# Kernel optimization log

Hardware: AMD Instinct MI355X
Metric: run time of the kernel (lower is better)

The kernel has to match this reference:

```python
import jax, jax.numpy as jnp
import numpy as np
from jax import lax

B = 32
NUM_CLASSES = 80
NUM_ANCHORS = 3
IMG_SIZE = 320
STRIDES = (8, 16, 32)
TOPK = 1000
CONF_THRESH = 0.05
NMS_THRESH = 0.6
EPS = 1e-10

ANCHOR_SIZES = np.array([[16, 16], [32, 32], [64, 48],
                         [64, 64], [96, 96], [128, 96],
                         [128, 128], [192, 160], [256, 256]],
                        dtype=np.float32).reshape(3, NUM_ANCHORS, 2)


def _build_anchors():
    # mirrors YOWOv3.generate_anchors
    boxes, strides = [], []
    for lvl, s in enumerate(STRIDES):
        f = IMG_SIZE // s
        ys, xs = np.meshgrid(np.arange(f), np.arange(f), indexing='ij')
        xy = np.stack([xs, ys], axis=-1).astype(np.float32).reshape(-1, 1, 2)
        xy = np.repeat(xy, NUM_ANCHORS, axis=1) * s            # [f*f, A, 2]
        wh = np.broadcast_to(ANCHOR_SIZES[lvl], (f * f, NUM_ANCHORS, 2))
        boxes.append(np.concatenate([xy, wh], axis=-1).reshape(-1, 4))
        strides.append(np.full(f * f * NUM_ANCHORS, s, dtype=np.float32))
    return np.concatenate(boxes, 0), np.concatenate(strides, 0)


def setup_inputs() -> dict:
    key = jax.random.key(0)
    k1, k2, k3 = jax.random.split(key, 3)
    anchors_np, stride_np = _build_anchors()
    M = anchors_np.shape[0]  # 6300
    conf_pred = jax.random.normal(k1, (B, M, 1), dtype=jnp.float32)
    cls_pred = jax.random.normal(k2, (B, M, NUM_CLASSES), dtype=jnp.float32) * 2.0
    reg_pred = jax.random.normal(k3, (B, M, 4), dtype=jnp.float32) * 0.5
    return {
        'conf_pred': conf_pred,
        'cls_pred': cls_pred,
        'reg_pred': reg_pred,
        'anchors': jnp.asarray(anchors_np),
        'stride_map': jnp.asarray(stride_np),
    }


def _decode_boxes(anchors, stride_map, reg_pred):
    # anchors [M,4] (cx, cy, w, h) in pixels; reg_pred [B,M,4]
    ctr = anchors[None, :, :2] + jax.nn.sigmoid(reg_pred[..., :2]) * stride_map[None, :, None]
    wh = anchors[None, :, 2:] * jnp.exp(reg_pred[..., 2:])
    return jnp.concatenate([ctr - 0.5 * wh, ctr + 0.5 * wh], axis=-1)  # [B,M,4] x1y1x2y2


def _nms_keep(boxes, scores, labels):
    # boxes [K,4] sorted by descending score; per-class greedy NMS -> bool keep [K]
    x1, y1, x2, y2 = boxes[:, 0], boxes[:, 1], boxes[:, 2], boxes[:, 3]
    areas = (x2 - x1) * (y2 - y1)
    xx1 = jnp.maximum(x1[:, None], x1[None, :])
    yy1 = jnp.maximum(y1[:, None], y1[None, :])
    xx2 = jnp.minimum(x2[:, None], x2[None, :])
    yy2 = jnp.minimum(y2[:, None], y2[None, :])
    inter = jnp.maximum(EPS, xx2 - xx1) * jnp.maximum(EPS, yy2 - yy1)
    union = jnp.maximum(areas[:, None] + areas[None, :] - inter, EPS)
    iou = inter / union
    suppress = (iou > NMS_THRESH) & (labels[:, None] == labels[None, :])
    keep0 = scores >= CONF_THRESH
    idxs = jnp.arange(boxes.shape[0])

    def body(i, keep):
        # if box i is kept, suppress all later same-class boxes with iou > thresh
        return keep & ~(keep[i] & suppress[i] & (idxs > i))

    return lax.fori_loop(0, boxes.shape[0], body, keep0)


def reference(conf_pred, cls_pred, reg_pred, anchors, stride_map):
    box_pred = _decode_boxes(anchors, stride_map, reg_pred)              # [B,M,4]
    joint = jax.nn.sigmoid(conf_pred) * jax.nn.softmax(cls_pred, -1)     # [B,M,C]
    scores = jnp.max(joint, axis=-1)                                     # [B,M]
    labels = jnp.argmax(joint, axis=-1)                                  # [B,M]

    top_scores, top_idx = lax.top_k(scores, TOPK)                        # sorted desc
    top_labels = jnp.take_along_axis(labels, top_idx, axis=1)
    top_boxes = jnp.take_along_axis(box_pred, top_idx[..., None], axis=1)
    top_boxes = jnp.clip(top_boxes / IMG_SIZE, 0.0, 1.0)                 # [B,K,4]

    keep = jax.vmap(_nms_keep)(top_boxes, top_scores, top_labels)        # [B,K] bool
    return top_scores, top_labels, top_boxes, keep
```

## Files before the change

kernel.cpp:

```cpp
#include <hip/hip_runtime.h>
#include <stdint.h>

#define NB 32
#define NM 6300
#define NC 80
#define NTOP 1000
#define NPAD 1024
#define NCAND 2048
#define NBINS 4096
#define BDT 1024

static constexpr float IMGSZ   = 320.0f;
static constexpr float CONF_TH = 0.05f;
static constexpr float NMS_TH  = 0.6f;
static constexpr float EPSF    = 1e-10f;

static constexpr size_t OFF_SCORES = 0;
static constexpr size_t OFF_LABELS = OFF_SCORES + (size_t)NB * NM * 4;
static constexpr size_t OFF_NBOX   = OFF_LABELS + (size_t)NB * NM * 4;
static constexpr size_t OFF_NLAB   = OFF_NBOX   + (size_t)NB * NPAD * 16;
static constexpr size_t OFF_SUP    = ((OFF_NLAB + (size_t)NB * NPAD * 4) + 1023) & ~(size_t)1023;

__global__ __launch_bounds__(256) void k_score(const float* __restrict__ conf,
                                               const float* __restrict__ cls,
                                               float* __restrict__ scores,
                                               int* __restrict__ labels) {
#pragma clang fp contract(off)
    int t = blockIdx.x * blockDim.x + threadIdx.x;
    int a = t >> 4;
    int l = t & 15;
    if (a >= NB * NM) return;
    const float* row = cls + (size_t)a * NC;

    float v[5];
#pragma unroll
    for (int k = 0; k < 5; ++k) v[k] = row[l + 16 * k];

    float bv = v[0];
    int bi = l;
#pragma unroll
    for (int k = 1; k < 5; ++k) {
        int c = l + 16 * k;
        if (v[k] > bv) { bv = v[k]; bi = c; }
    }
#pragma unroll
    for (int m = 1; m < 16; m <<= 1) {
        float ov = __shfl_xor(bv, m, 16);
        int   oi = __shfl_xor(bi, m, 16);
        if (ov > bv || (ov == bv && oi < bi)) { bv = ov; bi = oi; }
    }
    float s = 0.0f;
#pragma unroll
    for (int k = 0; k < 5; ++k) s += expf(v[k] - bv);
#pragma unroll
    for (int m = 1; m < 16; m <<= 1) s += __shfl_xor(s, m, 16);

    if (l == 0) {
        float cf  = conf[a];
        float sig = 1.0f / (1.0f + expf(-cf));
        float inv = 1.0f / s;
        scores[a] = sig * inv;
        labels[a] = bi;
    }
}

__global__ __launch_bounds__(BDT) void k_topk(const float* __restrict__ scores,
                                              const int* __restrict__ labels,
                                              const float* __restrict__ reg,
                                              const float* __restrict__ anchors,
                                              const float* __restrict__ stridemap,
                                              float* __restrict__ out_scores,
                                              float* __restrict__ out_labels,
                                              float* __restrict__ out_boxes,
                                              float* __restrict__ nbox,
                                              int* __restrict__ nlab) {
#pragma clang fp contract(off)
    __shared__ uint32_t hist[NBINS];
    __shared__ uint64_t key[NCAND];
    __shared__ int scnt;
    __shared__ int sT;
    int b = blockIdx.x, tid = threadIdx.x;
    const float* sb = scores + (size_t)b * NM;

    for (int i = tid; i < NBINS; i += BDT) hist[i] = 0;
    for (int i = tid; i < NCAND; i += BDT) key[i] = 0;
    if (tid == 0) scnt = 0;
    __syncthreads();

    for (int i = tid; i < NM; i += BDT)
        atomicAdd(&hist[__float_as_uint(sb[i]) >> 20], 1u);
    __syncthreads();

    if (tid < 64) {
        int l = tid;
        uint32_t q = 0;
        for (int i = 0; i < 64; ++i) q += hist[l * 64 + i];
        uint32_t s = q;
        for (int off = 1; off < 64; off <<= 1) {
            uint32_t o = __shfl_down(s, off);
            if (l + off < 64) s += o;
        }
        uint64_t m = __ballot(s >= (uint32_t)NTOP);
        int c = 63 - __clzll(m);
        uint32_t sc_ = __shfl(s, c);
        uint32_t qc  = __shfl(q, c);
        uint32_t tail = sc_ - qc;
        uint32_t v = hist[c * 64 + l];
        uint32_t s2 = v;
        for (int off = 1; off < 64; off <<= 1) {
            uint32_t o = __shfl_down(s2, off);
            if (l + off < 64) s2 += o;
        }
        uint64_t m2 = __ballot(s2 + tail >= (uint32_t)NTOP);
        int T = c * 64 + (63 - __clzll(m2));
        if (l == 0) sT = T;
    }
    __syncthreads();

    uint32_t T = (uint32_t)sT;
    int lane = tid & 63;
    for (int i = tid; i < NM; i += BDT) {
        uint32_t bits = __float_as_uint(sb[i]);
        bool pred = (bits >> 20) >= T;
        uint64_t mask = __ballot(pred);
        if (pred) {
            int leader = __ffsll((unsigned long long)mask) - 1;
            int prefix = __popcll(mask & ((1ull << lane) - 1));
            int base = 0;
            if (lane == leader) base = atomicAdd(&scnt, (int)__popcll(mask));
            base = __shfl(base, leader);
            int pos = base + prefix;
            if (pos < NCAND)
                key[pos] = ((uint64_t)bits << 32) | (uint32_t)(~(uint32_t)i);
        }
    }
    __syncthreads();

    uint64_t e0 = key[tid];
    uint64_t e1 = key[tid + 1024];

#pragma unroll
    for (int kk = 2; kk <= NCAND; kk <<= 1) {
#pragma unroll
        for (int j = kk >> 1; j > 0; j >>= 1) {
            if (j == 1024) {
                uint64_t mx = (e0 >= e1) ? e0 : e1;
                uint64_t mn = (e0 >= e1) ? e1 : e0;
                e0 = mx; e1 = mn;
            } else if (j >= 64) {
                __syncthreads();
                key[tid] = e0; key[tid + 1024] = e1;
                __syncthreads();
                uint64_t o0 = key[tid ^ j];
                uint64_t o1 = key[(tid + 1024) ^ j];
                bool lo  = ((tid & j) == 0);
                bool up0 = ((tid & kk) == 0);
                bool up1 = (((tid + 1024) & kk) == 0);
                e0 = (lo == up0) ? ((e0 >= o0) ? e0 : o0) : ((e0 >= o0) ? o0 : e0);
                e1 = (lo == up1) ? ((e1 >= o1) ? e1 : o1) : ((e1 >= o1) ? o1 : e1);
            } else {
                uint64_t o0 = __shfl_xor((unsigned long long)e0, j);
                uint64_t o1 = __shfl_xor((unsigned long long)e1, j);
                bool lo  = ((lane & j) == 0);
                bool up0 = ((tid & kk) == 0);
                bool up1 = (((tid + 1024) & kk) == 0);
                e0 = (lo == up0) ? ((e0 >= o0) ? e0 : o0) : ((e0 >= o0) ? o0 : e0);
                e1 = (lo == up1) ? ((e1 >= o1) ? e1 : o1) : ((e1 >= o1) ? o1 : e1);
            }
        }
    }

    if (tid < NTOP) {
        uint32_t sbits = (uint32_t)(e0 >> 32);
        int idx = (int)(~(uint32_t)e0);
        out_scores[b * NTOP + tid] = __uint_as_float(sbits);
        int lab = labels[(size_t)b * NM + idx];
        out_labels[b * NTOP + tid] = (float)lab;

        const float* rg = reg + ((size_t)b * NM + idx) * 4;
        float rx = rg[0], ry = rg[1], rw = rg[2], rh = rg[3];
        const float* an = anchors + (size_t)idx * 4;
        float ax = an[0], ay = an[1], aw = an[2], ah = an[3];
        float st = stridemap[idx];

        float sx = 1.0f / (1.0f + expf(-rx));
        float sy = 1.0f / (1.0f + expf(-ry));
        float cx = ax + sx * st;
        float cy = ay + sy * st;
        float w  = aw * expf(rw);
        float h  = ah * expf(rh);
        float x1 = cx - 0.5f * w, y1 = cy - 0.5f * h;
        float x2 = cx + 0.5f * w, y2 = cy + 0.5f * h;

        float nx1 = fminf(fmaxf(x1 / IMGSZ, 0.0f), 1.0f);
        float ny1 = fminf(fmaxf(y1 / IMGSZ, 0.0f), 1.0f);
        float nx2 = fminf(fmaxf(x2 / IMGSZ, 0.0f), 1.0f);
        float ny2 = fminf(fmaxf(y2 / IMGSZ, 0.0f), 1.0f);

        float4 bx = make_float4(nx1, ny1, nx2, ny2);
        ((float4*)out_boxes)[b * NTOP + tid] = bx;
        ((float4*)nbox)[b * NPAD + tid]      = bx;
        nlab[b * NPAD + tid] = lab;
    }
}

__global__ __launch_bounds__(256) void k_supmat(const float* __restrict__ nbox,
                                                const int* __restrict__ nlab,
                                                uint64_t* __restrict__ sup) {
#pragma clang fp contract(off)
    int b = blockIdx.y;
    int t = blockIdx.x;
    int tj = (int)((sqrtf(8.0f * (float)t + 1.0f) - 1.0f) * 0.5f);
    while ((tj + 1) * (tj + 2) / 2 <= t) ++tj;
    while (tj * (tj + 1) / 2 > t) --tj;
    int ti = t - tj * (tj + 1) / 2;

    int lane = threadIdx.x & 63;
    int w    = threadIdx.x >> 6;

    int i = ti * 64 + lane;
    int j = tj * 64 + lane;

    float4 bi = ((const float4*)nbox)[b * NPAD + i];
    float  ai = (bi.z - bi.x) * (bi.w - bi.y);
    int    li = nlab[b * NPAD + i];
    float4 bj = ((const float4*)nbox)[b * NPAD + j];
    int    lj = nlab[b * NPAD + j];
    bool   iv = (i < NTOP);

    uint64_t mybits = 0;
#pragma unroll
    for (int u = 0; u < 16; ++u) {
        int jj = (w << 4) | u;
        float bjx = __shfl(bj.x, jj);
        float bjy = __shfl(bj.y, jj);
        float bjz = __shfl(bj.z, jj);
        float bjw = __shfl(bj.w, jj);
        int   ljv = __shfl(lj, jj);
        float ajv = (bjz - bjx) * (bjw - bjy);
        int   jg  = tj * 64 + jj;
        float xx1 = fmaxf(bi.x, bjx);
        float yy1 = fmaxf(bi.y, bjy);
        float xx2 = fminf(bi.z, bjz);
        float yy2 = fminf(bi.w, bjw);
        float inter = fmaxf(EPSF, xx2 - xx1) * fmaxf(EPSF, yy2 - yy1);
        float uni   = fmaxf(ai + ajv - inter, EPSF);
        float iou   = inter / uni;
        bool pred = (i < jg) && iv && (jg < NTOP) && (li == ljv) && (iou > NMS_TH);
        uint64_t bal = __ballot(pred);
        if (lane == jj) mybits = bal;
    }
    if ((lane >> 4) == w)
        sup[(((size_t)b * 16 + tj) * 16 + ti) * 64 + lane] = mybits;
}

__global__ __launch_bounds__(1024) void k_nms(const float* __restrict__ out_scores,
                                              const uint64_t* __restrict__ sup,
                                              float* __restrict__ out_keep) {
    __shared__ uint64_t Kw[16];
    int b    = blockIdx.x;
    int w    = threadIdx.x >> 6;
    int lane = threadIdx.x & 63;
    const uint64_t* supb = sup + (size_t)b * 16 * 16 * 64;

    uint64_t wrow[16];
#pragma unroll
    for (int ti = 0; ti < 16; ++ti)
        wrow[ti] = (ti <= w) ? supb[((size_t)w * 16 + ti) * 64 + lane] : 0ULL;

    int pos = w * 64 + lane;
    bool k0 = (pos < NTOP) && (out_scores[b * NTOP + pos] >= CONF_TH);

    uint64_t ext = 0;
#pragma unroll
    for (int s = 0; s < 16; ++s) {
        if (w == s) {
            bool cand = k0 && (ext == 0ULL);
            uint64_t wself = wrow[s];
            uint64_t alive = __ballot(cand);
            for (int it = 0; it < 64; ++it) {
                bool dead = (wself & alive) != 0ULL;
                uint64_t na = __ballot(cand && !dead);
                if (na == alive) break;
                alive = na;
            }
            if (lane == 0) Kw[s] = alive;
            if (pos < NTOP)
                out_keep[b * NTOP + pos] = ((alive >> lane) & 1ULL) ? 1.0f : 0.0f;
        }
        __syncthreads();
        if (w > s) ext |= wrow[s] & Kw[s];
    }
}

extern "C" void kernel_launch(void* const* d_in, const int* in_sizes, int n_in,
                              void* d_out, int out_size, void* d_ws, size_t ws_size,
                              hipStream_t stream) {
    const float* conf = (const float*)d_in[0];
    const float* cls  = (const float*)d_in[1];
    const float* reg  = (const float*)d_in[2];
    const float* anch = (const float*)d_in[3];
    const float* strm = (const float*)d_in[4];

    float* out        = (float*)d_out;
    float* out_scores = out;
    float* out_labels = out + NB * NTOP;
    float* out_boxes  = out + 2 * NB * NTOP;
    float* out_keep   = out + 2 * NB * NTOP + NB * NTOP * 4;

    char* ws = (char*)d_ws;
    float*    scores = (float*)(ws + OFF_SCORES);
    int*      labels = (int*)(ws + OFF_LABELS);
    float*    nbox   = (float*)(ws + OFF_NBOX);
    int*      nlab   = (int*)(ws + OFF_NLAB);
    uint64_t* sup    = (uint64_t*)(ws + OFF_SUP);

    k_score<<<(NB * NM * 16) / 256, 256, 0, stream>>>(conf, cls, scores, labels);
    k_topk<<<NB, BDT, 0, stream>>>(scores, labels, reg, anch, strm,
                                   out_scores, out_labels, out_boxes, nbox, nlab);
    k_supmat<<<dim3(136, NB), 256, 0, stream>>>(nbox, nlab, sup);
    k_nms<<<NB, 1024, 0, stream>>>(out_scores, sup, out_keep);
}
```

Measured before the change: 67.73 us.

## Replace bitonic sort in top-k with bucket-chain rank computation

The 2048-element bitonic sort after radix-histogram thresholding is replaced. The kernel now builds a suffix-sum over histogram bins and per-bin linked lists of candidates, and computes each candidate's exact rank as the suffix count plus a walk over its own bin's chain. This removes the many __syncthreads-heavy sort stages, but adds per-candidate linked-list traversal with scattered global reads. That traversal can be slow if many candidates share a bin, and because the lists are built with atomics the chain order is nondeterministic.

```diff
diff --git a/kernel.cpp b/kernel.cpp
--- a/kernel.cpp
+++ b/kernel.cpp
@@ -8,7 +8,6 @@
 #define NPAD 1024
 #define NCAND 2048
 #define NBINS 4096
-#define BDT 1024
 
 static constexpr float IMGSZ   = 320.0f;
 static constexpr float CONF_TH = 0.05f;
@@ -64,143 +63,119 @@
     }
 }
 
-__global__ __launch_bounds__(BDT) void k_topk(const float* __restrict__ scores,
-                                              const int* __restrict__ labels,
-                                              const float* __restrict__ reg,
-                                              const float* __restrict__ anchors,
-                                              const float* __restrict__ stridemap,
-                                              float* __restrict__ out_scores,
-                                              float* __restrict__ out_labels,
-                                              float* __restrict__ out_boxes,
-                                              float* __restrict__ nbox,
-                                              int* __restrict__ nlab) {
+__global__ __launch_bounds__(1024) void k_topk(const float* __restrict__ scores,
+                                               const int* __restrict__ labels,
+                                               const float* __restrict__ reg,
+                                               const float* __restrict__ anchors,
+                                               const float* __restrict__ stridemap,
+                                               float* __restrict__ out_scores,
+                                               float* __restrict__ out_labels,
+                                               float* __restrict__ out_boxes,
+                                               float* __restrict__ nbox,
+                                               int* __restrict__ nlab) {
 #pragma clang fp contract(off)
     __shared__ uint32_t hist[NBINS];
-    __shared__ uint64_t key[NCAND];
-    __shared__ int scnt;
-    __shared__ int sT;
+    __shared__ uint32_t suf[NBINS];
+    __shared__ int      binHead[NBINS];
+    __shared__ uint16_t nxt[NM];
+    __shared__ uint16_t candList[NCAND];
+    __shared__ uint32_t csuf[64];
+    __shared__ int sT, scnt;
+
     int b = blockIdx.x, tid = threadIdx.x;
     const float* sb = scores + (size_t)b * NM;
 
-    for (int i = tid; i < NBINS; i += BDT) hist[i] = 0;
-    for (int i = tid; i < NCAND; i += BDT) key[i] = 0;
+    for (int i = tid; i < NBINS; i += 1024) { hist[i] = 0; binHead[i] = -1; }
     if (tid == 0) scnt = 0;
     __syncthreads();
 
-    for (int i = tid; i < NM; i += BDT)
+    for (int i = tid; i < NM; i += 1024)
         atomicAdd(&hist[__float_as_uint(sb[i]) >> 20], 1u);
     __syncthreads();
 
     if (tid < 64) {
-        int l = tid;
-        uint32_t q = 0;
-        for (int i = 0; i < 64; ++i) q += hist[l * 64 + i];
-        uint32_t s = q;
+        uint32_t cs = 0;
+        for (int k = 0; k < 64; ++k) cs += hist[tid * 64 + k];
+        uint32_t s = cs;
         for (int off = 1; off < 64; off <<= 1) {
             uint32_t o = __shfl_down(s, off);
-            if (l + off < 64) s += o;
-        }
-        uint64_t m = __ballot(s >= (uint32_t)NTOP);
-        int c = 63 - __clzll(m);
-        uint32_t sc_ = __shfl(s, c);
-        uint32_t qc  = __shfl(q, c);
-        uint32_t tail = sc_ - qc;
-        uint32_t v = hist[c * 64 + l];
-        uint32_t s2 = v;
+            if (tid + off < 64) s += o;
+        }
+        csuf[tid] = s - cs;
+    }
+    __syncthreads();
+
+    int ln = tid & 63, wv = tid >> 6;
+    for (int c = wv; c < 64; c += 16) {
+        uint32_t h = hist[c * 64 + ln];
+        uint32_t s = h;
         for (int off = 1; off < 64; off <<= 1) {
-            uint32_t o = __shfl_down(s2, off);
-            if (l + off < 64) s2 += o;
-        }
-        uint64_t m2 = __ballot(s2 + tail >= (uint32_t)NTOP);
-        int T = c * 64 + (63 - __clzll(m2));
-        if (l == 0) sT = T;
-    }
-    __syncthreads();
-
+            uint32_t o = __shfl_down(s, off);
+            if (ln + off < 64) s += o;
+        }
+        uint32_t sufv = csuf[c] + (s - h);
+        suf[c * 64 + ln] = sufv;
+        if (sufv < (uint32_t)NTOP && sufv + h >= (uint32_t)NTOP)
+            sT = c * 64 + ln;
+    }
+    __syncthreads();
     uint32_t T = (uint32_t)sT;
-    int lane = tid & 63;
-    for (int i = tid; i < NM; i += BDT) {
+
+    for (int i = tid; i < NM; i += 1024) {
+        uint32_t bin = __float_as_uint(sb[i]) >> 20;
+        if (bin >= T) {
+            int prev = atomicExch(&binHead[bin], i);
+            nxt[i] = (uint16_t)(prev < 0 ? 0xFFFFu : (uint32_t)prev);
+            int p = atomicAdd(&scnt, 1);
+            if (p < NCAND) candList[p] = (uint16_t)i;
+        }
+    }
+    __syncthreads();
+
+    int C = scnt; if (C > NCAND) C = NCAND;
+    for (int c = tid; c < C; c += 1024) {
+        int i = candList[c];
         uint32_t bits = __float_as_uint(sb[i]);
-        bool pred = (bits >> 20) >= T;
-        uint64_t mask = __ballot(pred);
-        if (pred) {
-            int leader = __ffsll((unsigned long long)mask) - 1;
-            int prefix = __popcll(mask & ((1ull << lane) - 1));
-            int base = 0;
-            if (lane == leader) base = atomicAdd(&scnt, (int)__popcll(mask));
-            base = __shfl(base, leader);
-            int pos = base + prefix;
-            if (pos < NCAND)
-                key[pos] = ((uint64_t)bits << 32) | (uint32_t)(~(uint32_t)i);
-        }
-    }
-    __syncthreads();
-
-    uint64_t e0 = key[tid];
-    uint64_t e1 = key[tid + 1024];
-
-#pragma unroll
-    for (int kk = 2; kk <= NCAND; kk <<= 1) {
-#pragma unroll
-        for (int j = kk >> 1; j > 0; j >>= 1) {
-            if (j == 1024) {
-                uint64_t mx = (e0 >= e1) ? e0 : e1;
-                uint64_t mn = (e0 >= e1) ? e1 : e0;
-                e0 = mx; e1 = mn;
-            } else if (j >= 64) {
-                __syncthreads();
-                key[tid] = e0; key[tid + 1024] = e1;
-                __syncthreads();
-                uint64_t o0 = key[tid ^ j];
-                uint64_t o1 = key[(tid + 1024) ^ j];
-                bool lo  = ((tid & j) == 0);
-                bool up0 = ((tid & kk) == 0);
-                bool up1 = (((tid + 1024) & kk) == 0);
-                e0 = (lo == up0) ? ((e0 >= o0) ? e0 : o0) : ((e0 >= o0) ? o0 : e0);
-                e1 = (lo == up1) ? ((e1 >= o1) ? e1 : o1) : ((e1 >= o1) ? o1 : e1);
-            } else {
-                uint64_t o0 = __shfl_xor((unsigned long long)e0, j);
-                uint64_t o1 = __shfl_xor((unsigned long long)e1, j);
-                bool lo  = ((lane & j) == 0);
-                bool up0 = ((tid & kk) == 0);
-                bool up1 = (((tid + 1024) & kk) == 0);
-                e0 = (lo == up0) ? ((e0 >= o0) ? e0 : o0) : ((e0 >= o0) ? o0 : e0);
-                e1 = (lo == up1) ? ((e1 >= o1) ? e1 : o1) : ((e1 >= o1) ? o1 : e1);
+        uint32_t bin  = bits >> 20;
+        uint32_t rank = suf[bin];
+        for (int m = binHead[bin]; m >= 0; ) {
+            if (m != i) {
+                uint32_t mb = __float_as_uint(sb[m]);
+                if (mb > bits || (mb == bits && m < i)) ++rank;
             }
-        }
-    }
-
-    if (tid < NTOP) {
-        uint32_t sbits = (uint32_t)(e0 >> 32);
-        int idx = (int)(~(uint32_t)e0);
-        out_scores[b * NTOP + tid] = __uint_as_float(sbits);
-        int lab = labels[(size_t)b * NM + idx];
-        out_labels[b * NTOP + tid] = (float)lab;
-
-        const float* rg = reg + ((size_t)b * NM + idx) * 4;
-        float rx = rg[0], ry = rg[1], rw = rg[2], rh = rg[3];
-        const float* an = anchors + (size_t)idx * 4;
-        float ax = an[0], ay = an[1], aw = an[2], ah = an[3];
-        float st = stridemap[idx];
-
-        float sx = 1.0f / (1.0f + expf(-rx));
-        float sy = 1.0f / (1.0f + expf(-ry));
-        float cx = ax + sx * st;
-        float cy = ay + sy * st;
-        float w  = aw * expf(rw);
-        float h  = ah * expf(rh);
-        float x1 = cx - 0.5f * w, y1 = cy - 0.5f * h;
-        float x2 = cx + 0.5f * w, y2 = cy + 0.5f * h;
-
-        float nx1 = fminf(fmaxf(x1 / IMGSZ, 0.0f), 1.0f);
-        float ny1 = fminf(fmaxf(y1 / IMGSZ, 0.0f), 1.0f);
-        float nx2 = fminf(fmaxf(x2 / IMGSZ, 0.0f), 1.0f);
-        float ny2 = fminf(fmaxf(y2 / IMGSZ, 0.0f), 1.0f);
-
-        float4 bx = make_float4(nx1, ny1, nx2, ny2);
-        ((float4*)out_boxes)[b * NTOP + tid] = bx;
-        ((float4*)nbox)[b * NPAD + tid]      = bx;
-        nlab[b * NPAD + tid] = lab;
+            uint16_t nx = nxt[m];
+            m = (nx == 0xFFFFu) ? -1 : (int)nx;
+        }
+        if (rank < (uint32_t)NTOP) {
+            out_scores[b * NTOP + rank] = __uint_as_float(bits);
+            int lab = labels[(size_t)b * NM + i];
+            out_labels[b * NTOP + rank] = (float)lab;
+
+            const float* rg = reg + ((size_t)b * NM + i) * 4;
+            float rx = rg[0], ry = rg[1], rw = rg[2], rh = rg[3];
+            const float* an = anchors + (size_t)i * 4;
+            float ax = an[0], ay = an[1], aw = an[2], ah = an[3];
+            float st = stridemap[i];
+
+            float sx = 1.0f / (1.0f + expf(-rx));
+            float sy = 1.0f / (1.0f + expf(-ry));
+            float cx = ax + sx * st;
+            float cy = ay + sy * st;
+            float w  = aw * expf(rw);
+            float h  = ah * expf(rh);
+            float x1 = cx - 0.5f * w, y1 = cy - 0.5f * h;
+            float x2 = cx + 0.5f * w, y2 = cy + 0.5f * h;
+
+            float nx1 = fminf(fmaxf(x1 / IMGSZ, 0.0f), 1.0f);
+            float ny1 = fminf(fmaxf(y1 / IMGSZ, 0.0f), 1.0f);
+            float nx2 = fminf(fmaxf(x2 / IMGSZ, 0.0f), 1.0f);
+            float ny2 = fminf(fmaxf(y2 / IMGSZ, 0.0f), 1.0f);
+
+            float4 bx = make_float4(nx1, ny1, nx2, ny2);
+            ((float4*)out_boxes)[b * NTOP + rank] = bx;
+            ((float4*)nbox)[b * NPAD + rank]      = bx;
+            nlab[b * NPAD + rank] = lab;
+        }
     }
 }
 
@@ -316,8 +291,8 @@
     uint64_t* sup    = (uint64_t*)(ws + OFF_SUP);
 
     k_score<<<(NB * NM * 16) / 256, 256, 0, stream>>>(conf, cls, scores, labels);
-    k_topk<<<NB, BDT, 0, stream>>>(scores, labels, reg, anch, strm,
-                                   out_scores, out_labels, out_boxes, nbox, nlab);
+    k_topk<<<NB, 1024, 0, stream>>>(scores, labels, reg, anch, strm,
+                                    out_scores, out_labels, out_boxes, nbox, nlab);
     k_supmat<<<dim3(136, NB), 256, 0, stream>>>(nbox, nlab, sup);
     k_nms<<<NB, 1024, 0, stream>>>(out_scores, sup, out_keep);
 }
```

Result: slower. 132.9 us (+96.3%).
